# Kernel tuning notes

Hardware: AMD Instinct MI355X
Metric: run time of the kernel (lower is better)

Reference implementation:

```python
import jax, jax.numpy as jnp
import numpy as np

B, C, N, H = 4, 256, 1024, 8
D = C            # per-head q/k dim (out_channels defaults to in_channels)
DV = C           # per-head value/output dim (y_out_channels defaults to out_channels)


def setup_inputs() -> dict:
    key = jax.random.key(0)
    ks = jax.random.split(key, 10)
    s = 0.02
    return {
        "x": jax.random.normal(ks[0], (B, C, N), jnp.float32),
        "y": jax.random.normal(ks[1], (B, C, N), jnp.float32),
        "Wq": jax.random.normal(ks[2], (H * D, C), jnp.float32) * s,
        "bq": jnp.zeros((H * D,), jnp.float32),
        "Wk": jax.random.normal(ks[3], (H * D, C), jnp.float32) * s,
        "bk": jnp.zeros((H * D,), jnp.float32),
        "Wv": jax.random.normal(ks[4], (H * DV, C), jnp.float32) * s,
        "bv": jnp.zeros((H * DV,), jnp.float32),
        "Wp": jax.random.normal(ks[5], (DV, C), jnp.float32) * s,  # projection, bias=False
        "gamma": jax.random.uniform(ks[6], (H, 1, 1, 1), jnp.float32) + 0.001,
    }


def _pconv(t, W, b):
    # 1x1 conv1d: (O,C) x (B,C,N) -> (B,O,N)
    out = jnp.einsum('oc,bcn->bon', W, t)
    return out if b is None else out + b[None, :, None]


def reference(x, y, Wq, bq, Wk, bk, Wv, bv, Wp, gamma):
    b_, _, n_ = x.shape
    h = gamma.shape[0]
    # Q/K/V projections, split channels into h heads (head-major chunks of D)
    q = _pconv(x, Wq, bq).reshape(b_, h, -1, n_)   # [B,H,D,N]
    k = _pconv(x, Wk, bk).reshape(b_, h, -1, n_)   # [B,H,D,N]
    v = _pconv(y, Wv, bv).reshape(b_, h, -1, n_)   # [B,H,DV,N]
    # energy[i,j] = sum_d q[d,i]*k[d,j]; softmax over keys j (no sqrt(d) scaling)
    attn = jax.nn.softmax(jnp.einsum('bhdn,bhdm->bhnm', q, k), axis=-1)
    out = jnp.einsum('bhdm,bhnm->bhdn', v, attn)   # [B,H,DV,N]
    # residual branch: y projected to DV channels (1x1 conv, no bias)
    yp = jnp.einsum('oc,bcn->bon', Wp, y)          # [B,DV,N]
    g = gamma.reshape(1, h, 1, 1)
    out = (g * out + yp[:, None, :, :]) / (1.0 + g)
    # concat heads along channel dim (head-major), matching split_cat(out,1,0,2)
    return out.reshape(b_, -1, n_)                 # [B,H*DV,N]
```

## Files before the change

### kernel.cpp

```cpp
#include <hip/hip_runtime.h>

#define Bb 4
#define Cc 256
#define Nn 1024
#define Hh 8
#define Oo 2048

typedef __attribute__((ext_vector_type(8))) short bf16x8;
typedef __attribute__((ext_vector_type(4))) float f32x4;

__device__ __forceinline__ short f2bf(float f) {
  unsigned u = __builtin_bit_cast(unsigned, f);
  unsigned r = u + 0x7FFFu + ((u >> 16) & 1u);
  return (short)(r >> 16);
}
__device__ __forceinline__ f32x4 mfma16(bf16x8 a, bf16x8 b, f32x4 c) {
  return __builtin_amdgcn_mfma_f32_16x16x32_bf16(a, b, c, 0, 0, 0);
}
__device__ __forceinline__ void gl_lds16(const void* g, void* l) {
  __builtin_amdgcn_global_load_lds(
      (const __attribute__((address_space(1))) void*)g,
      (__attribute__((address_space(3))) void*)l, 16, 0, 0);
}

__device__ __forceinline__ void stage_row512(const char* gbase, char* lds,
                                             int wave, int lane) {
#pragma unroll
  for (int i = 0; i < 8; i++) {
    int off = (wave * 8 + i) * 1024;
    int L = off + lane * 16;
    int r = L >> 9;
    int c = ((L >> 4) & 31) ^ (r & 7);
    gl_lds16(gbase + r * 512 + c * 16, lds + off);
  }
}
__device__ __forceinline__ void stage_v(const char* Vg, char* lds, int k0,
                                        int wave, int lane) {
#pragma unroll
  for (int i = 0; i < 8; i++) {
    int off = (wave * 8 + i) * 1024;
    int L = off + lane * 16;
    int r = L >> 7;
    int c = ((L >> 4) & 7) ^ (r & 7);
    gl_lds16(Vg + (size_t)r * 2048 + k0 * 2 + c * 16, lds + off);
  }
}

__global__ __launch_bounds__(256) void k_transpose(
    const float* __restrict__ x, const float* __restrict__ y,
    short* __restrict__ xT, short* __restrict__ yT,
    const float* __restrict__ Wq, const float* __restrict__ Wk,
    const float* __restrict__ Wv, const float* __restrict__ Wp,
    short* __restrict__ dWq, short* __restrict__ dWk, short* __restrict__ dWv,
    short* __restrict__ dWp) {
  {
    const int NW = Oo * Cc;
    int lin = blockIdx.x + 16 * (blockIdx.y + 4 * blockIdx.z);
    for (int i = (lin * 256 + threadIdx.x) * 4; i < 3 * NW + Cc * Cc;
         i += 512 * 256 * 4) {
      const float* src;
      short* dst;
      int off;
      if (i < NW) {
        src = Wq; dst = dWq; off = i;
      } else if (i < 2 * NW) {
        src = Wk; dst = dWk; off = i - NW;
      } else if (i < 3 * NW) {
        src = Wv; dst = dWv; off = i - 2 * NW;
      } else {
        src = Wp; dst = dWp; off = i - 3 * NW;
      }
      float4 v = *(const float4*)(src + off);
      short4 o;
      o.x = f2bf(v.x);
      o.y = f2bf(v.y);
      o.z = f2bf(v.z);
      o.w = f2bf(v.w);
      *(short4*)(dst + off) = o;
    }
  }
  int bz = blockIdx.z;
  int b = bz >> 1;
  const float* src = (bz & 1) ? y : x;
  short* dst = (bz & 1) ? yT : xT;
  src += (size_t)b * Cc * Nn;
  dst += (size_t)b * Nn * Cc;
  __shared__ short tile[64][72];
  int n0 = blockIdx.x * 64, c0 = blockIdx.y * 64;
  int t = threadIdx.x;
#pragma unroll
  for (int i = 0; i < 16; i++) {
    int idx = t + i * 256;
    int cc = idx >> 6, nn = idx & 63;
    tile[cc][nn] = f2bf(src[(size_t)(c0 + cc) * Nn + n0 + nn]);
  }
  __syncthreads();
#pragma unroll
  for (int i = 0; i < 16; i++) {
    int idx = t + i * 256;
    int nn = idx >> 6, cc = idx & 63;
    dst[(size_t)(n0 + nn) * Cc + c0 + cc] = tile[cc][nn];
  }
}

__global__ __launch_bounds__(256) void k_proj_qk(
    const short* __restrict__ xT, const short* __restrict__ Wq,
    const float* __restrict__ bq, const short* __restrict__ Wk,
    const float* __restrict__ bk, short* __restrict__ Qt,
    short* __restrict__ Kt) {
  int b = blockIdx.z, n0 = blockIdx.x * 64, o0 = blockIdx.y * 64;
  int wave = threadIdx.x >> 6, lane = threadIdx.x & 63;
  int quad = lane >> 4, l16 = lane & 15;
  int sw = l16 & 7;
  __shared__ short Wqs[64 * 256];
  __shared__ short Wks[64 * 256];

  stage_row512((const char*)(Wq + (size_t)o0 * Cc), (char*)Wqs, wave, lane);
  stage_row512((const char*)(Wk + (size_t)o0 * Cc), (char*)Wks, wave, lane);
  const short* aptr =
      xT + (size_t)b * Nn * Cc + (size_t)(n0 + wave * 16 + l16) * Cc + quad * 8;
  bf16x8 areg[8];
#pragma unroll
  for (int ks = 0; ks < 8; ks++) areg[ks] = *(const bf16x8*)(aptr + ks * 32);

  f32x4 accQ[4], accK[4];
#pragma unroll
  for (int j = 0; j < 4; j++) {
    accQ[j] = f32x4{0.f, 0.f, 0.f, 0.f};
    accK[j] = f32x4{0.f, 0.f, 0.f, 0.f};
  }
  __syncthreads();
#pragma unroll
  for (int ks = 0; ks < 8; ks++) {
#pragma unroll
    for (int cj = 0; cj < 4; cj++) {
      int off = (cj * 16 + l16) * 512 + (((ks * 4 + quad) ^ sw) << 4);
      bf16x8 wqf = *(const bf16x8*)((const char*)Wqs + off);
      bf16x8 wkf = *(const bf16x8*)((const char*)Wks + off);
      accQ[cj] = mfma16(areg[ks], wqf, accQ[cj]);
      accK[cj] = mfma16(areg[ks], wkf, accK[cj]);
    }
  }
#pragma unroll
  for (int cj = 0; cj < 4; cj++) {
    int o = o0 + cj * 16 + l16;
    int h = o >> 8, d = o & 255;
    float vbq = bq[o];
    float vbk = bk[o];
#pragma unroll
    for (int r = 0; r < 4; r++) {
      int n = n0 + wave * 16 + quad * 4 + r;
      size_t idx = (((size_t)(b * Hh + h) * Nn) + n) * 256 + d;
      Qt[idx] = f2bf(accQ[cj][r] + vbq);
      Kt[idx] = f2bf(accK[cj][r] + vbk);
    }
  }
}

__global__ __launch_bounds__(256) void k_proj_v(
    const short* __restrict__ yTs, const short* __restrict__ Wv,
    const float* __restrict__ bv, const short* __restrict__ Wp,
    short* __restrict__ Vv, float* __restrict__ yp) {
  int b = blockIdx.z, n0 = blockIdx.x * 64;
  int by = blockIdx.y;
  bool isP = by >= 32;
  const short* W = isP ? Wp : Wv;
  int o0 = (isP ? (by - 32) : by) * 64;
  int wave = threadIdx.x >> 6, lane = threadIdx.x & 63;
  int quad = lane >> 4, l16 = lane & 15;
  int sw = l16 & 7;
  __shared__ short Ys[64 * 256];

  stage_row512((const char*)(yTs + (size_t)b * Nn * Cc + (size_t)n0 * Cc),
               (char*)Ys, wave, lane);
  const short* aptr = W + (size_t)(o0 + wave * 16 + l16) * Cc + quad * 8;
  bf16x8 areg[8];
#pragma unroll
  for (int ks = 0; ks < 8; ks++) areg[ks] = *(const bf16x8*)(aptr + ks * 32);

  f32x4 acc[4];
#pragma unroll
  for (int j = 0; j < 4; j++) acc[j] = f32x4{0.f, 0.f, 0.f, 0.f};
  __syncthreads();
#pragma unroll
  for (int ks = 0; ks < 8; ks++) {
#pragma unroll
    for (int cj = 0; cj < 4; cj++) {
      bf16x8 bb = *(const bf16x8*)((const char*)Ys + (cj * 16 + l16) * 512 +
                                   (((ks * 4 + quad) ^ sw) << 4));
      acc[cj] = mfma16(areg[ks], bb, acc[cj]);
    }
  }
#pragma unroll
  for (int cj = 0; cj < 4; cj++) {
    int n = n0 + cj * 16 + l16;
#pragma unroll
    for (int r = 0; r < 4; r++) {
      int o = o0 + wave * 16 + quad * 4 + r;
      if (isP) {
        yp[((size_t)b * Cc + o) * Nn + n] = acc[cj][r];
      } else {
        float v = acc[cj][r] + bv[o];
        Vv[((size_t)b * Oo + o) * Nn + n] = f2bf(v);
      }
    }
  }
}

__global__ __launch_bounds__(256) void k_attn(
    const short* __restrict__ Qt, const short* __restrict__ Kt,
    const short* __restrict__ Vv, const float* __restrict__ yp,
    const float* __restrict__ gamma, float* __restrict__ out) {
  int id = blockIdx.x;
  int bh = (id & 7) * 4 + (id >> 7);
  int q0 = ((id >> 3) & 15) * 64;
  int b = bh >> 3, h = bh & 7;
  int wave = threadIdx.x >> 6, lane = threadIdx.x & 63;
  int quad = lane >> 4, l16 = lane & 15;
  int sw = l16 & 7;
  const short* Qb = Qt + (size_t)bh * Nn * 256;
  const char* Kg = (const char*)(Kt + (size_t)bh * Nn * 256);
  const char* Vg = (const char*)(Vv + (size_t)bh * 256 * Nn);

  __shared__ short Klds[64 * 256];
  __shared__ short Vlds[256 * 64];
  __shared__ short plds[4][16][64];
  __shared__ float llds[64];

  bf16x8 qreg[8];
  {
    const short* qp = Qb + (size_t)(q0 + wave * 16 + l16) * 256 + quad * 8;
#pragma unroll
    for (int ks = 0; ks < 8; ks++) qreg[ks] = *(const bf16x8*)(qp + ks * 32);
  }
  f32x4 oacc[16];
#pragma unroll
  for (int j = 0; j < 16; j++) oacc[j] = f32x4{0.f, 0.f, 0.f, 0.f};
  float l_i[4] = {0.f, 0.f, 0.f, 0.f};

  stage_row512(Kg, (char*)Klds, wave, lane);
  stage_v(Vg, (char*)Vlds, 0, wave, lane);

  for (int kt = 0; kt < 16; kt++) {
    int k0 = kt * 64;
    __syncthreads();
    f32x4 sc[4];
#pragma unroll
    for (int j = 0; j < 4; j++) sc[j] = f32x4{0.f, 0.f, 0.f, 0.f};
#pragma unroll
    for (int ks = 0; ks < 8; ks++) {
#pragma unroll
      for (int cj = 0; cj < 4; cj++) {
        bf16x8 kb = *(const bf16x8*)((const char*)Klds +
                                     (cj * 16 + l16) * 512 +
                                     (((ks * 4 + quad) ^ sw) << 4));
        sc[cj] = mfma16(qreg[ks], kb, sc[cj]);
      }
    }
#pragma unroll
    for (int cj = 0; cj < 4; cj++) {
#pragma unroll
      for (int r = 0; r < 4; r++) {
        float p = __expf(sc[cj][r]);
        l_i[r] += p;
        int row = quad * 4 + r;
        plds[wave][row][(((cj * 2 + (l16 >> 3)) ^ (row & 7)) << 3) | sw] =
            f2bf(p);
      }
    }
    __syncthreads();
    if (kt < 15)
      stage_row512(Kg + (size_t)(k0 + 64) * 512, (char*)Klds, wave, lane);
    bf16x8 ap0[4], ap1[4];
#pragma unroll
    for (int qb = 0; qb < 4; qb++) {
      ap0[qb] = *(const bf16x8*)&plds[qb][l16][(quad ^ sw) << 3];
      ap1[qb] = *(const bf16x8*)&plds[qb][l16][((quad + 4) ^ sw) << 3];
    }
#pragma unroll
    for (int dj = 0; dj < 4; dj++) {
      const char* vrow = (const char*)Vlds + (wave * 64 + dj * 16 + l16) * 128;
      bf16x8 v0 = *(const bf16x8*)(vrow + ((quad ^ sw) << 4));
      bf16x8 v1 = *(const bf16x8*)(vrow + (((quad + 4) ^ sw) << 4));
#pragma unroll
      for (int qb = 0; qb < 4; qb++) {
        oacc[qb * 4 + dj] = mfma16(ap0[qb], v0, oacc[qb * 4 + dj]);
        oacc[qb * 4 + dj] = mfma16(ap1[qb], v1, oacc[qb * 4 + dj]);
      }
    }
    __syncthreads();
    if (kt < 15) stage_v(Vg, (char*)Vlds, k0 + 64, wave, lane);
  }
#pragma unroll
  for (int r = 0; r < 4; r++) {
    float v = l_i[r];
    v += __shfl_xor(v, 1);
    v += __shfl_xor(v, 2);
    v += __shfl_xor(v, 4);
    v += __shfl_xor(v, 8);
    l_i[r] = v;
  }
  if (l16 == 0) {
    f32x4 lv;
#pragma unroll
    for (int r = 0; r < 4; r++) lv[r] = l_i[r];
    *(f32x4*)&llds[wave * 16 + quad * 4] = lv;
  }
  __syncthreads();
  float gf = gamma[h];
  float sg = gf / (1.f + gf), sy = 1.f / (1.f + gf);
#pragma unroll
  for (int qb = 0; qb < 4; qb++) {
    f32x4 lv = *(const f32x4*)&llds[qb * 16 + quad * 4];
    int qq = q0 + qb * 16 + quad * 4;
#pragma unroll
    for (int dj = 0; dj < 4; dj++) {
      int dv = wave * 64 + dj * 16 + l16;
      const float* ypp = yp + ((size_t)b * 256 + dv) * Nn + qq;
      float* op = out + ((size_t)b * Oo + h * 256 + dv) * Nn + qq;
      float4 yv = *(const float4*)ypp;
      f32x4 oa = oacc[qb * 4 + dj];
      float4 ov;
      ov.x = sg * (oa[0] / lv[0]) + sy * yv.x;
      ov.y = sg * (oa[1] / lv[1]) + sy * yv.y;
      ov.z = sg * (oa[2] / lv[2]) + sy * yv.z;
      ov.w = sg * (oa[3] / lv[3]) + sy * yv.w;
      *(float4*)op = ov;
    }
  }
}

extern "C" void kernel_launch(void* const* d_in, const int* in_sizes, int n_in,
                              void* d_out, int out_size, void* d_ws,
                              size_t ws_size, hipStream_t stream) {
  const float* x = (const float*)d_in[0];
  const float* y = (const float*)d_in[1];
  const float* Wq = (const float*)d_in[2];
  const float* bq = (const float*)d_in[3];
  const float* Wk = (const float*)d_in[4];
  const float* bk = (const float*)d_in[5];
  const float* Wv = (const float*)d_in[6];
  const float* bv = (const float*)d_in[7];
  const float* Wp = (const float*)d_in[8];
  const float* gamma = (const float*)d_in[9];
  float* out = (float*)d_out;

  char* w = (char*)d_ws;
  short* Qt = (short*)(w + 0);
  short* Kt = (short*)(w + 16777216);
  short* Vv = (short*)(w + 33554432);
  short* xT = (short*)(w + 50331648);
  short* yT = (short*)(w + 52428800);
  float* yp = (float*)(w + 54525952);
  short* Wqb = (short*)(w + 58720256);
  short* Wkb = (short*)(w + 59768832);
  short* Wvb = (short*)(w + 60817408);
  short* Wpb = (short*)(w + 61865984);

  k_transpose<<<dim3(Nn / 64, Cc / 64, 2 * Bb), dim3(256), 0, stream>>>(
      x, y, xT, yT, Wq, Wk, Wv, Wp, Wqb, Wkb, Wvb, Wpb);
  k_proj_qk<<<dim3(Nn / 64, Oo / 64, Bb), dim3(256), 0, stream>>>(
      xT, Wqb, bq, Wkb, bk, Qt, Kt);
  k_proj_v<<<dim3(Nn / 64, 36, Bb), dim3(256), 0, stream>>>(yT, Wvb, bv, Wpb,
                                                            Vv, yp);
  k_attn<<<dim3(512), dim3(256), 0, stream>>>(Qt, Kt, Vv, yp, gamma, out);
}
```

Baseline: 183.6 us.

## Merge QK and V projection kernels into one launch using 32x32 MFMA tiles

```diff
diff --git a/kernel.cpp b/kernel.cpp
--- a/kernel.cpp
+++ b/kernel.cpp
@@ -8,6 +8,7 @@
 
 typedef __attribute__((ext_vector_type(8))) short bf16x8;
 typedef __attribute__((ext_vector_type(4))) float f32x4;
+typedef __attribute__((ext_vector_type(16))) float f32x16;
 
 __device__ __forceinline__ short f2bf(float f) {
   unsigned u = __builtin_bit_cast(unsigned, f);
@@ -16,6 +17,9 @@
 }
 __device__ __forceinline__ f32x4 mfma16(bf16x8 a, bf16x8 b, f32x4 c) {
   return __builtin_amdgcn_mfma_f32_16x16x32_bf16(a, b, c, 0, 0, 0);
+}
+__device__ __forceinline__ f32x16 mfma32(bf16x8 a, bf16x8 b, f32x16 c) {
+  return __builtin_amdgcn_mfma_f32_32x32x16_bf16(a, b, c, 0, 0, 0);
 }
 __device__ __forceinline__ void gl_lds16(const void* g, void* l) {
   __builtin_amdgcn_global_load_lds(
@@ -103,105 +107,79 @@
   }
 }
 
-__global__ __launch_bounds__(256) void k_proj_qk(
-    const short* __restrict__ xT, const short* __restrict__ Wq,
-    const float* __restrict__ bq, const short* __restrict__ Wk,
-    const float* __restrict__ bk, short* __restrict__ Qt,
-    short* __restrict__ Kt) {
-  int b = blockIdx.z, n0 = blockIdx.x * 64, o0 = blockIdx.y * 64;
+__global__ __launch_bounds__(256) void k_proj(
+    const short* __restrict__ xT, const short* __restrict__ yT,
+    const short* __restrict__ Wq, const float* __restrict__ bq,
+    const short* __restrict__ Wk, const float* __restrict__ bk,
+    const short* __restrict__ Wv, const float* __restrict__ bv,
+    const short* __restrict__ Wp, short* __restrict__ Qt,
+    short* __restrict__ Kt, short* __restrict__ Vv, float* __restrict__ yp) {
+  int b = blockIdx.z, n0 = blockIdx.x * 64, by = blockIdx.y;
   int wave = threadIdx.x >> 6, lane = threadIdx.x & 63;
-  int quad = lane >> 4, l16 = lane & 15;
-  int sw = l16 & 7;
-  __shared__ short Wqs[64 * 256];
-  __shared__ short Wks[64 * 256];
-
-  stage_row512((const char*)(Wq + (size_t)o0 * Cc), (char*)Wqs, wave, lane);
-  stage_row512((const char*)(Wk + (size_t)o0 * Cc), (char*)Wks, wave, lane);
-  const short* aptr =
-      xT + (size_t)b * Nn * Cc + (size_t)(n0 + wave * 16 + l16) * Cc + quad * 8;
-  bf16x8 areg[8];
-#pragma unroll
-  for (int ks = 0; ks < 8; ks++) areg[ks] = *(const bf16x8*)(aptr + ks * 32);
-
-  f32x4 accQ[4], accK[4];
-#pragma unroll
-  for (int j = 0; j < 4; j++) {
-    accQ[j] = f32x4{0.f, 0.f, 0.f, 0.f};
-    accK[j] = f32x4{0.f, 0.f, 0.f, 0.f};
-  }
-  __syncthreads();
-#pragma unroll
-  for (int ks = 0; ks < 8; ks++) {
-#pragma unroll
-    for (int cj = 0; cj < 4; cj++) {
-      int off = (cj * 16 + l16) * 512 + (((ks * 4 + quad) ^ sw) << 4);
-      bf16x8 wqf = *(const bf16x8*)((const char*)Wqs + off);
-      bf16x8 wkf = *(const bf16x8*)((const char*)Wks + off);
-      accQ[cj] = mfma16(areg[ks], wqf, accQ[cj]);
-      accK[cj] = mfma16(areg[ks], wkf, accK[cj]);
-    }
-  }
-#pragma unroll
-  for (int cj = 0; cj < 4; cj++) {
-    int o = o0 + cj * 16 + l16;
+  int l32 = lane & 31, half = lane >> 5, sw = lane & 7;
+  int nh = wave >> 1, oh = wave & 1;
+  __shared__ short Ws[2][64 * 256];
+
+  if (by < 32) {
+    stage_row512((const char*)(Wq + (size_t)by * 64 * Cc), (char*)Ws[0], wave,
+                 lane);
+    stage_row512((const char*)(Wk + (size_t)by * 64 * Cc), (char*)Ws[1], wave,
+                 lane);
+  } else if (by < 64) {
+    stage_row512((const char*)(Wv + (size_t)(by - 32) * 64 * Cc), (char*)Ws[0],
+                 wave, lane);
+  } else {
+    stage_row512((const char*)(Wp + (size_t)(by - 64) * 64 * Cc), (char*)Ws[0],
+                 wave, lane);
+  }
+
+  const short* rbase = (by < 32 ? xT : yT) +
+                       ((size_t)b * Nn + n0 + nh * 32 + l32) * Cc + half * 8;
+  bf16x8 rreg[16];
+#pragma unroll
+  for (int s = 0; s < 16; s++) rreg[s] = *(const bf16x8*)(rbase + s * 16);
+
+  if (by < 32) {
+    f32x16 accQ = {}, accK = {};
+    __syncthreads();
+#pragma unroll
+    for (int s = 0; s < 16; s++) {
+      int woff = (oh * 32 + l32) * 512 + (((s * 2 + half) ^ sw) << 4);
+      bf16x8 wq = *(const bf16x8*)((const char*)Ws[0] + woff);
+      bf16x8 wk = *(const bf16x8*)((const char*)Ws[1] + woff);
+      accQ = mfma32(rreg[s], wq, accQ);
+      accK = mfma32(rreg[s], wk, accK);
+    }
+    int o = by * 64 + oh * 32 + l32;
     int h = o >> 8, d = o & 255;
-    float vbq = bq[o];
-    float vbk = bk[o];
-#pragma unroll
-    for (int r = 0; r < 4; r++) {
-      int n = n0 + wave * 16 + quad * 4 + r;
-      size_t idx = (((size_t)(b * Hh + h) * Nn) + n) * 256 + d;
-      Qt[idx] = f2bf(accQ[cj][r] + vbq);
-      Kt[idx] = f2bf(accK[cj][r] + vbk);
-    }
-  }
-}
-
-__global__ __launch_bounds__(256) void k_proj_v(
-    const short* __restrict__ yTs, const short* __restrict__ Wv,
-    const float* __restrict__ bv, const short* __restrict__ Wp,
-    short* __restrict__ Vv, float* __restrict__ yp) {
-  int b = blockIdx.z, n0 = blockIdx.x * 64;
-  int by = blockIdx.y;
-  bool isP = by >= 32;
-  const short* W = isP ? Wp : Wv;
-  int o0 = (isP ? (by - 32) : by) * 64;
-  int wave = threadIdx.x >> 6, lane = threadIdx.x & 63;
-  int quad = lane >> 4, l16 = lane & 15;
-  int sw = l16 & 7;
-  __shared__ short Ys[64 * 256];
-
-  stage_row512((const char*)(yTs + (size_t)b * Nn * Cc + (size_t)n0 * Cc),
-               (char*)Ys, wave, lane);
-  const short* aptr = W + (size_t)(o0 + wave * 16 + l16) * Cc + quad * 8;
-  bf16x8 areg[8];
-#pragma unroll
-  for (int ks = 0; ks < 8; ks++) areg[ks] = *(const bf16x8*)(aptr + ks * 32);
-
-  f32x4 acc[4];
-#pragma unroll
-  for (int j = 0; j < 4; j++) acc[j] = f32x4{0.f, 0.f, 0.f, 0.f};
-  __syncthreads();
-#pragma unroll
-  for (int ks = 0; ks < 8; ks++) {
-#pragma unroll
-    for (int cj = 0; cj < 4; cj++) {
-      bf16x8 bb = *(const bf16x8*)((const char*)Ys + (cj * 16 + l16) * 512 +
-                                   (((ks * 4 + quad) ^ sw) << 4));
-      acc[cj] = mfma16(areg[ks], bb, acc[cj]);
-    }
-  }
-#pragma unroll
-  for (int cj = 0; cj < 4; cj++) {
-    int n = n0 + cj * 16 + l16;
-#pragma unroll
-    for (int r = 0; r < 4; r++) {
-      int o = o0 + wave * 16 + quad * 4 + r;
+    float vbq = bq[o], vbk = bk[o];
+    size_t rowbase = (size_t)(b * Hh + h) * Nn;
+#pragma unroll
+    for (int reg = 0; reg < 16; reg++) {
+      int m = (reg & 3) + 8 * (reg >> 2) + 4 * half;
+      size_t idx = (rowbase + n0 + nh * 32 + m) * 256 + d;
+      Qt[idx] = f2bf(accQ[reg] + vbq);
+      Kt[idx] = f2bf(accK[reg] + vbk);
+    }
+  } else {
+    bool isP = by >= 64;
+    int o0 = (isP ? (by - 64) : (by - 32)) * 64;
+    f32x16 acc = {};
+    __syncthreads();
+#pragma unroll
+    for (int s = 0; s < 16; s++) {
+      int woff = (oh * 32 + l32) * 512 + (((s * 2 + half) ^ sw) << 4);
+      bf16x8 wf = *(const bf16x8*)((const char*)Ws[0] + woff);
+      acc = mfma32(wf, rreg[s], acc);
+    }
+    int n = n0 + nh * 32 + l32;
+#pragma unroll
+    for (int reg = 0; reg < 16; reg++) {
+      int o = o0 + oh * 32 + (reg & 3) + 8 * (reg >> 2) + 4 * half;
       if (isP) {
-        yp[((size_t)b * Cc + o) * Nn + n] = acc[cj][r];
+        yp[((size_t)b * Cc + o) * Nn + n] = acc[reg];
       } else {
-        float v = acc[cj][r] + bv[o];
-        Vv[((size_t)b * Oo + o) * Nn + n] = f2bf(v);
+        Vv[((size_t)b * Oo + o) * Nn + n] = f2bf(acc[reg] + bv[o]);
       }
     }
   }
@@ -359,9 +337,7 @@
 
   k_transpose<<<dim3(Nn / 64, Cc / 64, 2 * Bb), dim3(256), 0, stream>>>(
       x, y, xT, yT, Wq, Wk, Wv, Wp, Wqb, Wkb, Wvb, Wpb);
-  k_proj_qk<<<dim3(Nn / 64, Oo / 64, Bb), dim3(256), 0, stream>>>(
-      xT, Wqb, bq, Wkb, bk, Qt, Kt);
-  k_proj_v<<<dim3(Nn / 64, 36, Bb), dim3(256), 0, stream>>>(yT, Wvb, bv, Wpb,
-                                                            Vv, yp);
+  k_proj<<<dim3(Nn / 64, 68, Bb), dim3(256), 0, stream>>>(
+      xT, yT, Wqb, bq, Wkb, bk, Wvb, bv, Wpb, Qt, Kt, Vv, yp);
   k_attn<<<dim3(512), dim3(256), 0, stream>>>(Qt, Kt, Vv, yp, gamma, out);
 }
```

After: 204.7 us. 11.5% more time.

## Load V tiles directly into registers with double buffering instead of LDS

Applied to the files above, without the earlier changes.

```diff
diff --git a/kernel.cpp b/kernel.cpp
--- a/kernel.cpp
+++ b/kernel.cpp
@@ -32,17 +32,6 @@
     int r = L >> 9;
     int c = ((L >> 4) & 31) ^ (r & 7);
     gl_lds16(gbase + r * 512 + c * 16, lds + off);
-  }
-}
-__device__ __forceinline__ void stage_v(const char* Vg, char* lds, int k0,
-                                        int wave, int lane) {
-#pragma unroll
-  for (int i = 0; i < 8; i++) {
-    int off = (wave * 8 + i) * 1024;
-    int L = off + lane * 16;
-    int r = L >> 7;
-    int c = ((L >> 4) & 7) ^ (r & 7);
-    gl_lds16(Vg + (size_t)r * 2048 + k0 * 2 + c * 16, lds + off);
   }
 }
 
@@ -220,10 +209,9 @@
   int sw = l16 & 7;
   const short* Qb = Qt + (size_t)bh * Nn * 256;
   const char* Kg = (const char*)(Kt + (size_t)bh * Nn * 256);
-  const char* Vg = (const char*)(Vv + (size_t)bh * 256 * Nn);
+  const short* Vb = Vv + (size_t)bh * 256 * Nn;
 
   __shared__ short Klds[64 * 256];
-  __shared__ short Vlds[256 * 64];
   __shared__ short plds[4][16][64];
   __shared__ float llds[64];
 
@@ -238,12 +226,28 @@
   for (int j = 0; j < 16; j++) oacc[j] = f32x4{0.f, 0.f, 0.f, 0.f};
   float l_i[4] = {0.f, 0.f, 0.f, 0.f};
 
+  const short* vbase = Vb + (size_t)(wave * 64 + l16) * Nn + quad * 8;
+
+  bf16x8 vA[8], vB[8];
+#pragma unroll
+  for (int dj = 0; dj < 4; dj++) {
+    const short* vp = vbase + (size_t)(dj * 16) * Nn;
+    vA[dj * 2] = *(const bf16x8*)vp;
+    vA[dj * 2 + 1] = *(const bf16x8*)(vp + 32);
+  }
   stage_row512(Kg, (char*)Klds, wave, lane);
-  stage_v(Vg, (char*)Vlds, 0, wave, lane);
-
-  for (int kt = 0; kt < 16; kt++) {
+
+  auto iter = [&](int kt, bf16x8 (&vcur)[8], bf16x8 (&vnxt)[8]) {
     int k0 = kt * 64;
     __syncthreads();
+    if (kt < 15) {
+#pragma unroll
+      for (int dj = 0; dj < 4; dj++) {
+        const short* vp = vbase + (size_t)(dj * 16) * Nn + k0 + 64;
+        vnxt[dj * 2] = *(const bf16x8*)vp;
+        vnxt[dj * 2 + 1] = *(const bf16x8*)(vp + 32);
+      }
+    }
     f32x4 sc[4];
 #pragma unroll
     for (int j = 0; j < 4; j++) sc[j] = f32x4{0.f, 0.f, 0.f, 0.f};
@@ -279,18 +283,21 @@
     }
 #pragma unroll
     for (int dj = 0; dj < 4; dj++) {
-      const char* vrow = (const char*)Vlds + (wave * 64 + dj * 16 + l16) * 128;
-      bf16x8 v0 = *(const bf16x8*)(vrow + ((quad ^ sw) << 4));
-      bf16x8 v1 = *(const bf16x8*)(vrow + (((quad + 4) ^ sw) << 4));
 #pragma unroll
       for (int qb = 0; qb < 4; qb++) {
-        oacc[qb * 4 + dj] = mfma16(ap0[qb], v0, oacc[qb * 4 + dj]);
-        oacc[qb * 4 + dj] = mfma16(ap1[qb], v1, oacc[qb * 4 + dj]);
-      }
-    }
-    __syncthreads();
-    if (kt < 15) stage_v(Vg, (char*)Vlds, k0 + 64, wave, lane);
-  }
+        oacc[qb * 4 + dj] = mfma16(ap0[qb], vcur[dj * 2], oacc[qb * 4 + dj]);
+        oacc[qb * 4 + dj] =
+            mfma16(ap1[qb], vcur[dj * 2 + 1], oacc[qb * 4 + dj]);
+      }
+    }
+  };
+
+#pragma unroll 1
+  for (int kt2 = 0; kt2 < 8; kt2++) {
+    iter(kt2 * 2, vA, vB);
+    iter(kt2 * 2 + 1, vB, vA);
+  }
+
 #pragma unroll
   for (int r = 0; r < 4; r++) {
     float v = l_i[r];
```

Measured after the change: 204.6 us. +11.4%, slower.
